# Performance work log

Measured on AMD Instinct MI355X. Metric: run time of the kernel, lower is better.

## Reference

```python
import jax, jax.numpy as jnp
import numpy as np

DIM = 1024
NUM_HEADS = 16


def setup_inputs() -> dict:
    key = jax.random.key(0)
    ks = jax.random.split(key, 8)
    B, N, C = 2, 2048, DIM
    x = jax.random.normal(ks[0], (B, N, C), dtype=jnp.float32)
    attn_mask = jnp.zeros((B, 1, N, N), dtype=jnp.float32)
    # learned parameters
    w_qkv = jax.random.normal(ks[1], (3 * C, C), dtype=jnp.float32) * (C ** -0.5)
    q_bias = jnp.zeros((C,), dtype=jnp.float32)
    k_bias = jnp.zeros((C,), dtype=jnp.float32)
    v_bias = jnp.zeros((C,), dtype=jnp.float32)
    w_proj = jax.random.normal(ks[2], (C, C), dtype=jnp.float32) * (C ** -0.5)
    b_proj = jnp.zeros((C,), dtype=jnp.float32)
    return {
        "x": x, "attn_mask": attn_mask,
        "w_qkv": w_qkv, "q_bias": q_bias, "k_bias": k_bias, "v_bias": v_bias,
        "w_proj": w_proj, "b_proj": b_proj,
        "num_heads": NUM_HEADS,
    }


def reference(x, attn_mask, w_qkv, q_bias, k_bias, v_bias, w_proj, b_proj, num_heads):
    B, N, C = x.shape
    H = num_heads
    hd = C // H
    scale = hd ** -0.5
    alpha = 32.0
    # fused qkv projection with concatenated biases
    qkv_bias = jnp.concatenate([q_bias, k_bias, v_bias])
    qkv = x @ w_qkv.T + qkv_bias                       # [B, N, 3C]
    qkv = qkv.reshape(B, N, 3, H, hd).transpose(2, 0, 3, 1, 4)  # [3, B, H, N, hd]
    q, k, v = qkv[0], qkv[1], qkv[2]
    # stabilization trick: scale q down by alpha, compute scores, re-scale after max-subtraction
    q = q * (scale / alpha)
    attn = jnp.einsum('bhld,bhmd->bhlm', q, k)         # [B, H, N, N]
    attn = (attn - jnp.max(attn, axis=-1, keepdims=True)) * alpha
    attn = attn + attn_mask                            # additive mask, broadcast over heads
    attn = jax.nn.softmax(attn, axis=-1)
    out = jnp.einsum('bhlm,bhmd->blhd', attn, v).reshape(B, N, C)
    out = out @ w_proj.T + b_proj
    return out
```

## Files before the change

### kernel.cpp

```cpp
#include <hip/hip_runtime.h>

typedef unsigned short u16;
typedef __bf16   bf16x8 __attribute__((ext_vector_type(8)));
typedef float    f32x4  __attribute__((ext_vector_type(4)));
typedef float    f32x16 __attribute__((ext_vector_type(16)));
typedef unsigned u32x4v __attribute__((ext_vector_type(4)));
typedef u16      u16x8  __attribute__((ext_vector_type(8)));

#define DEV __device__ __forceinline__

DEV u16 tobf(float f) {
  return __builtin_bit_cast(unsigned short, (__bf16)f);
}

DEV unsigned pack2(float a, float b) {
  return (unsigned)tobf(a) | ((unsigned)tobf(b) << 16);
}

DEV f32x4 fzero() { f32x4 z; z[0]=0.f; z[1]=0.f; z[2]=0.f; z[3]=0.f; return z; }

DEV void async_cp16(void* lds, const void* g) {
  __builtin_amdgcn_global_load_lds(
      (const __attribute__((address_space(1))) void*)g,
      (__attribute__((address_space(3))) void*)lds, 16, 0, 0);
}

DEV void cvt8(const float* __restrict__ in, u16* __restrict__ out, int i) {
  const float4* in4 = (const float4*)in;
  float4 a = in4[2*i], b = in4[2*i+1];
  u16x8 r;
  r[0]=tobf(a.x); r[1]=tobf(a.y); r[2]=tobf(a.z); r[3]=tobf(a.w);
  r[4]=tobf(b.x); r[5]=tobf(b.y); r[6]=tobf(b.z); r[7]=tobf(b.w);
  *(u16x8*)(out + 8*(size_t)i) = r;
}

__global__ void k_zero_flag(unsigned* f) {
  if (threadIdx.x == 0 && blockIdx.x == 0) *f = 0u;
}

__global__ __launch_bounds__(256)
void k_pre(const float* __restrict__ x, const float* __restrict__ wqkv,
           const float* __restrict__ wproj,
           u16* __restrict__ xb, u16* __restrict__ wqkvb, u16* __restrict__ wprojb,
           const u32x4v* __restrict__ mask, unsigned* __restrict__ flag)
{
  const int tid = blockIdx.x * blockDim.x + threadIdx.x;
  const int stride = gridDim.x * blockDim.x;
  for (int i = tid; i < 524288; i += stride) cvt8(x, xb, i);
  for (int i = tid; i < 393216; i += stride) cvt8(wqkv, wqkvb, i);
  for (int i = tid; i < 131072; i += stride) cvt8(wproj, wprojb, i);
  unsigned o = 0;
  for (int i = tid; i < 2097152; i += stride) {
    u32x4v v = mask[i];
    o |= v[0] | v[1] | v[2] | v[3];
  }
  if (o & 0x7fffffffu) atomicOr(flag, 1u);
}

template<int EPI>
__global__ __launch_bounds__(256)
void k_gemm_nt(const u16* __restrict__ A, const u16* __restrict__ B,
               int N, int K, int nbn,
               const float* __restrict__ bq, const float* __restrict__ bk,
               const float* __restrict__ bv,
               u16* __restrict__ qo, u16* __restrict__ ko, u16* __restrict__ vto,
               float* __restrict__ fo, const float* __restrict__ bp)
{
  __shared__ u16 sA[2][4096];
  __shared__ u16 sB[2][4096];

  const int tid  = threadIdx.x;
  const int lane = tid & 63;
  const int wave = tid >> 6;
  const int lr = lane & 15, lg = lane >> 4;
  const int wr = wave >> 1, wc = wave & 1;

  const int per = gridDim.x >> 3;
  const int bid = blockIdx.x;
  const int swz = (bid & 7) * per + (bid >> 3);
  const int bm0 = (swz / nbn) << 7;
  const int bn0 = (swz - (swz / nbn) * nbn) << 7;

  const size_t Kb = (size_t)K * 2;

  auto stage = [&](int buf, int kt) {
#pragma unroll
    for (int j = 0; j < 2; ++j) {
      int off = (tid + j * 256) << 4;
      int row = off >> 6;
      int ch  = (off & 63) >> 4;
      int gch = ch ^ (row & 3);
      async_cp16((char*)&sA[buf][0] + off,
                 (const char*)A + (size_t)(bm0 + row) * Kb + (size_t)kt * 64 + gch * 16);
      async_cp16((char*)&sB[buf][0] + off,
                 (const char*)B + (size_t)(bn0 + row) * Kb + (size_t)kt * 64 + gch * 16);
    }
  };

  f32x4 acc[4][4];
#pragma unroll
  for (int i = 0; i < 4; ++i)
#pragma unroll
    for (int j = 0; j < 4; ++j) acc[i][j] = fzero();

  const int nk = K >> 5;
  stage(0, 0);
  __syncthreads();

  for (int kt = 0; kt < nk; ++kt) {
    const int cur = kt & 1;
    if (kt + 1 < nk) stage(cur ^ 1, kt + 1);

    bf16x8 af[4], bfr[4];
#pragma unroll
    for (int mi = 0; mi < 4; ++mi) {
      int row = (wr << 6) + (mi << 4) + lr;
      int addr = (row << 6) + ((lg ^ (row & 3)) << 4);
      af[mi] = *(const bf16x8*)((const char*)&sA[cur][0] + addr);
    }
#pragma unroll
    for (int ni = 0; ni < 4; ++ni) {
      int row = (wc << 6) + (ni << 4) + lr;
      int addr = (row << 6) + ((lg ^ (row & 3)) << 4);
      bfr[ni] = *(const bf16x8*)((const char*)&sB[cur][0] + addr);
    }
#pragma unroll
    for (int mi = 0; mi < 4; ++mi)
#pragma unroll
      for (int ni = 0; ni < 4; ++ni)
        acc[mi][ni] = __builtin_amdgcn_mfma_f32_16x16x32_bf16(af[mi], bfr[ni], acc[mi][ni], 0, 0, 0);

    __syncthreads();
  }

#pragma unroll
  for (int mi = 0; mi < 4; ++mi) {
#pragma unroll
    for (int ni = 0; ni < 4; ++ni) {
      int col = bn0 + (wc << 6) + (ni << 4) + lr;
      if (EPI == 0) {
        int s = col >> 10, hd = col & 1023;
        int h = hd >> 6, d = hd & 63;
        float bias = (s == 0 ? bq[hd] : (s == 1 ? bk[hd] : bv[hd]));
#pragma unroll
        for (int r = 0; r < 4; ++r) {
          int m = bm0 + (wr << 6) + (mi << 4) + (lg << 2) + r;
          int b = m >> 11, n = m & 2047;
          float v = acc[mi][ni][r] + bias;
          if (s == 0) v *= 0.125f;
          u16 val = tobf(v);
          size_t bh = (size_t)(b * 16 + h);
          if (s == 0)      qo[(bh * 2048 + n) * 64 + d] = val;
          else if (s == 1) ko[(bh * 2048 + n) * 64 + d] = val;
          else             vto[(bh * 64 + d) * 2048 + n] = val;
        }
      } else {
        float bias = bp[col];
#pragma unroll
        for (int r = 0; r < 4; ++r) {
          int m = bm0 + (wr << 6) + (mi << 4) + (lg << 2) + r;
          fo[(size_t)m * N + col] = acc[mi][ni][r] + bias;
        }
      }
    }
  }
}

__global__ __launch_bounds__(256)
void k_attn(const u16* __restrict__ qb, const u16* __restrict__ kb,
            const u16* __restrict__ vtb, u16* __restrict__ ao,
            const float* __restrict__ mask, const unsigned* __restrict__ flag)
{
  constexpr int N = 2048;
  __shared__ u16 sK[2][4096];
  __shared__ u16 sV[2][4096];

  const int tid  = threadIdx.x;
  const int lane = tid & 63;
  const int wave = tid >> 6;
  const int l31  = lane & 31;
  const int hi   = lane >> 5;

  const int bid  = blockIdx.x;
  const int xcd  = bid & 7, slot = bid >> 3;
  const int bh   = xcd + 8 * (slot >> 4);
  const int qt   = slot & 15;
  const int b    = bh >> 4, h = bh & 15;

  const u16* Kbh = kb  + (size_t)bh * N * 64;
  const u16* Vbh = vtb + (size_t)bh * 64 * N;
  const int q_lo = qt * 128 + wave * 32;
  const int qg   = q_lo + l31;

  bf16x8 qf[4];
  {
    const u16* qrow = qb + ((size_t)bh * N + qg) * 64;
#pragma unroll
    for (int ks = 0; ks < 4; ++ks)
      qf[ks] = *(const bf16x8*)(qrow + ks * 16 + hi * 8);
  }

  const unsigned use_mask = *flag;
  const float* maskb = mask + (size_t)b * N * N;

  float m_run = -INFINITY, lsum = 0.f;
  f32x16 o0, o1;
#pragma unroll
  for (int r = 0; r < 16; ++r) { o0[r] = 0.f; o1[r] = 0.f; }

  auto stage = [&](int buf, int kt) {
#pragma unroll
    for (int j = 0; j < 2; ++j) {
      int off = (tid + j * 256) << 4;
      int row = off >> 7;
      int ch  = (off & 127) >> 4;
      int gch = ch ^ (row & 7);
      async_cp16((char*)&sK[buf][0] + off,
                 (const char*)Kbh + (size_t)(kt * 64 + row) * 128 + gch * 16);
      async_cp16((char*)&sV[buf][0] + off,
                 (const char*)Vbh + (size_t)row * (N * 2) + (size_t)kt * 128 + gch * 16);
    }
  };

  stage(0, 0);
  __syncthreads();

  const float L2E = 1.44269504088896340736f;

  for (int kt = 0; kt < N / 64; ++kt) {
    const int cur = kt & 1;
    if (kt + 1 < N / 64) stage(cur ^ 1, kt + 1);

    f32x16 sc0, sc1;
#pragma unroll
    for (int r = 0; r < 16; ++r) { sc0[r] = 0.f; sc1[r] = 0.f; }

    __builtin_amdgcn_s_setprio(1);
#pragma unroll
    for (int ks = 0; ks < 4; ++ks) {
      int row0 = l31;
      int a0 = (row0 << 7) + ((((ks << 1) + hi) ^ (row0 & 7)) << 4);
      bf16x8 kf0 = *(const bf16x8*)((const char*)&sK[cur][0] + a0);
      sc0 = __builtin_amdgcn_mfma_f32_32x32x16_bf16(kf0, qf[ks], sc0, 0, 0, 0);
      int row1 = 32 + l31;
      int a1 = (row1 << 7) + ((((ks << 1) + hi) ^ (row1 & 7)) << 4);
      bf16x8 kf1 = *(const bf16x8*)((const char*)&sK[cur][0] + a1);
      sc1 = __builtin_amdgcn_mfma_f32_32x32x16_bf16(kf1, qf[ks], sc1, 0, 0, 0);
    }
    __builtin_amdgcn_s_setprio(0);

    if (use_mask) {
#pragma unroll
      for (int r = 0; r < 16; ++r) {
        int krow = (r & 3) + 8 * (r >> 2) + 4 * hi;
        sc0[r] += maskb[(size_t)qg * N + kt * 64 + krow];
        sc1[r] += maskb[(size_t)qg * N + kt * 64 + 32 + krow];
      }
    }

    float t[8];
#pragma unroll
    for (int r = 0; r < 8; ++r)
      t[r] = fmaxf(fmaxf(sc0[r], sc0[r + 8]), fmaxf(sc1[r], sc1[r + 8]));
#pragma unroll
    for (int r = 0; r < 4; ++r) t[r] = fmaxf(t[r], t[r + 4]);
    float pm = fmaxf(fmaxf(t[0], t[1]), fmaxf(t[2], t[3]));
    pm = fmaxf(pm, __shfl_xor(pm, 32, 64));

    if (__any(pm > m_run + 8.f)) {
      const float m_new = fmaxf(m_run, pm);
      const float f = __builtin_amdgcn_exp2f((m_run - m_new) * L2E);
      m_run = m_new;
      float fr[16];
#pragma unroll
      for (int r = 0; r < 16; ++r)
        fr[r] = __shfl(f, (r & 3) + 8 * (r >> 2) + 4 * hi, 64);
#pragma unroll
      for (int r = 0; r < 16; ++r) { o0[r] *= fr[r]; o1[r] *= fr[r]; }
      lsum *= f;
    }

    const float mL2 = m_run * L2E;
    float rs0 = 0.f, rs1 = 0.f, rs2 = 0.f, rs3 = 0.f;
#pragma unroll
    for (int r = 0; r < 16; r += 4) {
      sc0[r]   = __builtin_amdgcn_exp2f(__builtin_fmaf(sc0[r],   L2E, -mL2));
      sc0[r+1] = __builtin_amdgcn_exp2f(__builtin_fmaf(sc0[r+1], L2E, -mL2));
      sc0[r+2] = __builtin_amdgcn_exp2f(__builtin_fmaf(sc0[r+2], L2E, -mL2));
      sc0[r+3] = __builtin_amdgcn_exp2f(__builtin_fmaf(sc0[r+3], L2E, -mL2));
      sc1[r]   = __builtin_amdgcn_exp2f(__builtin_fmaf(sc1[r],   L2E, -mL2));
      sc1[r+1] = __builtin_amdgcn_exp2f(__builtin_fmaf(sc1[r+1], L2E, -mL2));
      sc1[r+2] = __builtin_amdgcn_exp2f(__builtin_fmaf(sc1[r+2], L2E, -mL2));
      sc1[r+3] = __builtin_amdgcn_exp2f(__builtin_fmaf(sc1[r+3], L2E, -mL2));
      rs0 += sc0[r]   + sc1[r];
      rs1 += sc0[r+1] + sc1[r+1];
      rs2 += sc0[r+2] + sc1[r+2];
      rs3 += sc0[r+3] + sc1[r+3];
    }
    float rs = (rs0 + rs1) + (rs2 + rs3);
    rs += __shfl_xor(rs, 32, 64);
    lsum += rs;

    unsigned P32_0[8], P32_1[8];
#pragma unroll
    for (int tt = 0; tt < 8; ++tt) {
      P32_0[tt] = pack2(sc0[2 * tt], sc0[2 * tt + 1]);
      P32_1[tt] = pack2(sc1[2 * tt], sc1[2 * tt + 1]);
    }

    bf16x8 pa[4];
#pragma unroll
    for (int ks16 = 0; ks16 < 4; ++ks16) {
      const int b4 = (ks16 & 1) << 2;
      unsigned c0, c1, c2, c3;
      if (ks16 < 2) { c0 = P32_0[b4]; c2 = P32_0[b4+2]; c1 = P32_0[b4+1]; c3 = P32_0[b4+3]; }
      else          { c0 = P32_1[b4]; c2 = P32_1[b4+2]; c1 = P32_1[b4+1]; c3 = P32_1[b4+3]; }
      asm volatile("v_permlane32_swap_b32 %0, %1" : "+v"(c0), "+v"(c2));
      asm volatile("v_permlane32_swap_b32 %0, %1" : "+v"(c1), "+v"(c3));
      u32x4v w; w[0] = c0; w[1] = c1; w[2] = c2; w[3] = c3;
      pa[ks16] = __builtin_bit_cast(bf16x8, w);
    }

    __builtin_amdgcn_s_setprio(1);
#pragma unroll
    for (int ks16 = 0; ks16 < 4; ++ks16) {
      int row0 = l31;
      int a0 = (row0 << 7) + ((((ks16 << 1) + hi) ^ (row0 & 7)) << 4);
      bf16x8 vf0 = *(const bf16x8*)((const char*)&sV[cur][0] + a0);
      o0 = __builtin_amdgcn_mfma_f32_32x32x16_bf16(pa[ks16], vf0, o0, 0, 0, 0);
      int row1 = 32 + l31;
      int a1 = (row1 << 7) + ((((ks16 << 1) + hi) ^ (row1 & 7)) << 4);
      bf16x8 vf1 = *(const bf16x8*)((const char*)&sV[cur][0] + a1);
      o1 = __builtin_amdgcn_mfma_f32_32x32x16_bf16(pa[ks16], vf1, o1, 0, 0, 0);
    }
    __builtin_amdgcn_s_setprio(0);

    __syncthreads();
  }

  const float inv = 1.0f / lsum;
  float ivr[16];
#pragma unroll
  for (int r = 0; r < 16; ++r)
    ivr[r] = __shfl(inv, (r & 3) + 8 * (r >> 2) + 4 * hi, 64);

#pragma unroll
  for (int r = 0; r < 16; ++r) {
    int qrow = q_lo + (r & 3) + 8 * (r >> 2) + 4 * hi;
    size_t base = ((size_t)(b * N + qrow)) * 1024 + h * 64;
    ao[base + l31]      = tobf(o0[r] * ivr[r]);
    ao[base + 32 + l31] = tobf(o1[r] * ivr[r]);
  }
}

extern "C" void kernel_launch(void* const* d_in, const int* in_sizes, int n_in,
                              void* d_out, int out_size, void* d_ws, size_t ws_size,
                              hipStream_t stream) {
  const float* x      = (const float*)d_in[0];
  const float* mask   = (const float*)d_in[1];
  const float* w_qkv  = (const float*)d_in[2];
  const float* q_bias = (const float*)d_in[3];
  const float* k_bias = (const float*)d_in[4];
  const float* v_bias = (const float*)d_in[5];
  const float* w_proj = (const float*)d_in[6];
  const float* b_proj = (const float*)d_in[7];
  float* out = (float*)d_out;

  const int B = 2, N = 2048, C = 1024;
  const int M = B * N;

  u16* ws     = (u16*)d_ws;
  u16* xb     = ws;
  u16* wqkvb  = ws + 4194304;
  u16* wprojb = ws + 7340032;
  u16* qbuf   = ws + 8388608;
  u16* kbuf   = ws + 12582912;
  u16* vtbuf  = ws + 16777216;
  unsigned* flag = (unsigned*)(ws + 20971520);
  u16* aob    = xb;

  k_zero_flag<<<1, 64, 0, stream>>>(flag);
  k_pre<<<2048, 256, 0, stream>>>(x, w_qkv, w_proj, xb, wqkvb, wprojb,
                                  (const u32x4v*)mask, flag);

  k_gemm_nt<0><<<(M / 128) * (3 * C / 128), 256, 0, stream>>>(
      xb, wqkvb, 3 * C, C, 3 * C / 128,
      q_bias, k_bias, v_bias, qbuf, kbuf, vtbuf, nullptr, nullptr);

  k_attn<<<B * 16 * (N / 128), 256, 0, stream>>>(qbuf, kbuf, vtbuf, aob, mask, flag);

  k_gemm_nt<1><<<(M / 128) * (C / 128), 256, 0, stream>>>(
      aob, wprojb, C, C, C / 128,
      nullptr, nullptr, nullptr, nullptr, nullptr, nullptr, out, b_proj);
}
```

Before: 143.1 us.

## Split KV loop across two wave groups per block and merge softmax partials

Attention blocks now use 512 threads as two groups of four waves, each processing alternating 64-key tiles with their own double-buffered K/V shared memory. At the end, group 1 writes its running max, sum and output accumulators to shared memory and group 0 merges them with rescaling before writing bf16 output. This aims to raise waves per CU and halve the sequential key loop length per wave, at the cost of doubled LDS usage and an extra merge step.

```diff
diff --git a/kernel.cpp b/kernel.cpp
--- a/kernel.cpp
+++ b/kernel.cpp
@@ -166,18 +166,22 @@
   }
 }
 
-__global__ __launch_bounds__(256)
+__global__ __launch_bounds__(512, 4)
 void k_attn(const u16* __restrict__ qb, const u16* __restrict__ kb,
             const u16* __restrict__ vtb, u16* __restrict__ ao,
             const float* __restrict__ mask, const unsigned* __restrict__ flag)
 {
   constexpr int N = 2048;
-  __shared__ u16 sK[2][4096];
-  __shared__ u16 sV[2][4096];
+  __shared__ u16 sK[2][2][4096];
+  __shared__ u16 sV[2][2][4096];
+  __shared__ float2 sStats[256];
 
   const int tid  = threadIdx.x;
   const int lane = tid & 63;
   const int wave = tid >> 6;
+  const int g    = wave >> 2;
+  const int wq   = wave & 3;
+  const int ltid = tid & 255;
   const int l31  = lane & 31;
   const int hi   = lane >> 5;
 
@@ -189,7 +193,7 @@
 
   const u16* Kbh = kb  + (size_t)bh * N * 64;
   const u16* Vbh = vtb + (size_t)bh * 64 * N;
-  const int q_lo = qt * 128 + wave * 32;
+  const int q_lo = qt * 128 + wq * 32;
   const int qg   = q_lo + l31;
 
   bf16x8 qf[4];
@@ -211,25 +215,29 @@
   auto stage = [&](int buf, int kt) {
 #pragma unroll
     for (int j = 0; j < 2; ++j) {
-      int off = (tid + j * 256) << 4;
+      int off = (ltid + j * 256) << 4;
       int row = off >> 7;
       int ch  = (off & 127) >> 4;
       int gch = ch ^ (row & 7);
-      async_cp16((char*)&sK[buf][0] + off,
+      async_cp16((char*)&sK[g][buf][0] + off,
                  (const char*)Kbh + (size_t)(kt * 64 + row) * 128 + gch * 16);
-      async_cp16((char*)&sV[buf][0] + off,
+      async_cp16((char*)&sV[g][buf][0] + off,
                  (const char*)Vbh + (size_t)row * (N * 2) + (size_t)kt * 128 + gch * 16);
     }
   };
 
-  stage(0, 0);
+  stage(0, g);
   __syncthreads();
 
   const float L2E = 1.44269504088896340736f;
 
-  for (int kt = 0; kt < N / 64; ++kt) {
-    const int cur = kt & 1;
-    if (kt + 1 < N / 64) stage(cur ^ 1, kt + 1);
+  for (int t = 0; t < 16; ++t) {
+    const int kt  = 2 * t + g;
+    const int cur = t & 1;
+    if (t + 1 < 16) stage(cur ^ 1, kt + 2);
+
+    const char* kbase = (const char*)&sK[g][cur][0];
+    const char* vbase = (const char*)&sV[g][cur][0];
 
     f32x16 sc0, sc1;
 #pragma unroll
@@ -240,11 +248,11 @@
     for (int ks = 0; ks < 4; ++ks) {
       int row0 = l31;
       int a0 = (row0 << 7) + ((((ks << 1) + hi) ^ (row0 & 7)) << 4);
-      bf16x8 kf0 = *(const bf16x8*)((const char*)&sK[cur][0] + a0);
+      bf16x8 kf0 = *(const bf16x8*)(kbase + a0);
       sc0 = __builtin_amdgcn_mfma_f32_32x32x16_bf16(kf0, qf[ks], sc0, 0, 0, 0);
       int row1 = 32 + l31;
       int a1 = (row1 << 7) + ((((ks << 1) + hi) ^ (row1 & 7)) << 4);
-      bf16x8 kf1 = *(const bf16x8*)((const char*)&sK[cur][0] + a1);
+      bf16x8 kf1 = *(const bf16x8*)(kbase + a1);
       sc1 = __builtin_amdgcn_mfma_f32_32x32x16_bf16(kf1, qf[ks], sc1, 0, 0, 0);
     }
     __builtin_amdgcn_s_setprio(0);
@@ -258,13 +266,13 @@
       }
     }
 
-    float t[8];
+    float tmx[8];
 #pragma unroll
     for (int r = 0; r < 8; ++r)
-      t[r] = fmaxf(fmaxf(sc0[r], sc0[r + 8]), fmaxf(sc1[r], sc1[r + 8]));
-#pragma unroll
-    for (int r = 0; r < 4; ++r) t[r] = fmaxf(t[r], t[r + 4]);
-    float pm = fmaxf(fmaxf(t[0], t[1]), fmaxf(t[2], t[3]));
+      tmx[r] = fmaxf(fmaxf(sc0[r], sc0[r + 8]), fmaxf(sc1[r], sc1[r + 8]));
+#pragma unroll
+    for (int r = 0; r < 4; ++r) tmx[r] = fmaxf(tmx[r], tmx[r + 4]);
+    float pm = fmaxf(fmaxf(tmx[0], tmx[1]), fmaxf(tmx[2], tmx[3]));
     pm = fmaxf(pm, __shfl_xor(pm, 32, 64));
 
     if (__any(pm > m_run + 8.f)) {
@@ -326,11 +334,11 @@
     for (int ks16 = 0; ks16 < 4; ++ks16) {
       int row0 = l31;
       int a0 = (row0 << 7) + ((((ks16 << 1) + hi) ^ (row0 & 7)) << 4);
-      bf16x8 vf0 = *(const bf16x8*)((const char*)&sV[cur][0] + a0);
+      bf16x8 vf0 = *(const bf16x8*)(vbase + a0);
       o0 = __builtin_amdgcn_mfma_f32_32x32x16_bf16(pa[ks16], vf0, o0, 0, 0, 0);
       int row1 = 32 + l31;
       int a1 = (row1 << 7) + ((((ks16 << 1) + hi) ^ (row1 & 7)) << 4);
-      bf16x8 vf1 = *(const bf16x8*)((const char*)&sV[cur][0] + a1);
+      bf16x8 vf1 = *(const bf16x8*)(vbase + a1);
       o1 = __builtin_amdgcn_mfma_f32_32x32x16_bf16(pa[ks16], vf1, o1, 0, 0, 0);
     }
     __builtin_amdgcn_s_setprio(0);
@@ -338,18 +346,47 @@
     __syncthreads();
   }
 
-  const float inv = 1.0f / lsum;
-  float ivr[16];
-#pragma unroll
-  for (int r = 0; r < 16; ++r)
-    ivr[r] = __shfl(inv, (r & 3) + 8 * (r >> 2) + 4 * hi, 64);
-
-#pragma unroll
-  for (int r = 0; r < 16; ++r) {
-    int qrow = q_lo + (r & 3) + 8 * (r >> 2) + 4 * hi;
-    size_t base = ((size_t)(b * N + qrow)) * 1024 + h * 64;
-    ao[base + l31]      = tobf(o0[r] * ivr[r]);
-    ao[base + 32 + l31] = tobf(o1[r] * ivr[r]);
+  const int sw = lane & 7;
+  {
+    float* R = (wq < 2) ? ((float*)&sK[1][0][0] + ((wq & 1) * 64 + lane) * 32)
+                        : ((float*)&sV[1][0][0] + ((wq & 1) * 64 + lane) * 32);
+    if (g == 1) {
+      sStats[wq * 64 + lane] = make_float2(m_run, lsum);
+#pragma unroll
+      for (int i = 0; i < 4; ++i) {
+        f32x4 tv; tv[0]=o0[4*i]; tv[1]=o0[4*i+1]; tv[2]=o0[4*i+2]; tv[3]=o0[4*i+3];
+        *(f32x4*)(R + 4 * (i ^ sw)) = tv;
+      }
+#pragma unroll
+      for (int i = 0; i < 4; ++i) {
+        f32x4 tv; tv[0]=o1[4*i]; tv[1]=o1[4*i+1]; tv[2]=o1[4*i+2]; tv[3]=o1[4*i+3];
+        *(f32x4*)(R + 4 * ((i + 4) ^ sw)) = tv;
+      }
+    }
+    __syncthreads();
+    if (g == 0) {
+      float2 s1 = sStats[wq * 64 + lane];
+      float mf = fmaxf(m_run, s1.x);
+      float ea = __builtin_amdgcn_exp2f((m_run - mf) * L2E);
+      float eb = __builtin_amdgcn_exp2f((s1.x  - mf) * L2E);
+      float lf = __builtin_fmaf(lsum, ea, s1.y * eb);
+      float ai = ea / lf, bi = eb / lf;
+      f32x4 c[8];
+#pragma unroll
+      for (int i = 0; i < 8; ++i) c[i] = *(const f32x4*)(R + 4 * (i ^ sw));
+#pragma unroll
+      for (int r = 0; r < 16; ++r) {
+        int idx = (r & 3) + 8 * (r >> 2) + 4 * hi;
+        float Ar = __shfl(ai, idx, 64);
+        float Br = __shfl(bi, idx, 64);
+        float v0 = __builtin_fmaf(o0[r], Ar, c[r >> 2][r & 3] * Br);
+        float v1 = __builtin_fmaf(o1[r], Ar, c[4 + (r >> 2)][r & 3] * Br);
+        int qrow = q_lo + idx;
+        size_t base = ((size_t)(b * N + qrow)) * 1024 + h * 64;
+        ao[base + l31]      = tobf(v0);
+        ao[base + 32 + l31] = tobf(v1);
+      }
+    }
   }
 }
 
@@ -387,7 +424,7 @@
       xb, wqkvb, 3 * C, C, 3 * C / 128,
       q_bias, k_bias, v_bias, qbuf, kbuf, vtbuf, nullptr, nullptr);
 
-  k_attn<<<B * 16 * (N / 128), 256, 0, stream>>>(qbuf, kbuf, vtbuf, aob, mask, flag);
+  k_attn<<<B * 16 * (N / 128), 512, 0, stream>>>(qbuf, kbuf, vtbuf, aob, mask, flag);
 
   k_gemm_nt<1><<<(M / 128) * (C / 128), 256, 0, stream>>>(
       aob, wprojb, C, C, C / 128,
```

After: 144.7 us. Within noise of the previous version (+1.1%).

## Restructure attention into single-wave blocks with 32-key tiles and no barriers

Applied to the files above, without the earlier changes.

The attention kernel now uses one 64-thread wave per block, each owning 32 query rows. It streams 32-key tiles through double-buffered LDS with a new swizzle for the half-width V tile, and syncs with explicit vmcnt waits instead of __syncthreads. The aim is to remove block-level barrier stalls and raise the number of independent waves. In exchange, K/V reuse across query tiles within a block is lost, global and L2 traffic rises, and each tile issues fewer MFMAs between synchronisation points. The flag-zeroing kernel is also replaced by hipMemsetAsync.

```diff
diff --git a/kernel.cpp b/kernel.cpp
--- a/kernel.cpp
+++ b/kernel.cpp
@@ -32,10 +32,6 @@
   r[0]=tobf(a.x); r[1]=tobf(a.y); r[2]=tobf(a.z); r[3]=tobf(a.w);
   r[4]=tobf(b.x); r[5]=tobf(b.y); r[6]=tobf(b.z); r[7]=tobf(b.w);
   *(u16x8*)(out + 8*(size_t)i) = r;
-}
-
-__global__ void k_zero_flag(unsigned* f) {
-  if (threadIdx.x == 0 && blockIdx.x == 0) *f = 0u;
 }
 
 __global__ __launch_bounds__(256)
@@ -166,30 +162,29 @@
   }
 }
 
-__global__ __launch_bounds__(256)
+__global__ __launch_bounds__(64)
 void k_attn(const u16* __restrict__ qb, const u16* __restrict__ kb,
             const u16* __restrict__ vtb, u16* __restrict__ ao,
             const float* __restrict__ mask, const unsigned* __restrict__ flag)
 {
   constexpr int N = 2048;
-  __shared__ u16 sK[2][4096];
-  __shared__ u16 sV[2][4096];
-
-  const int tid  = threadIdx.x;
-  const int lane = tid & 63;
-  const int wave = tid >> 6;
+  constexpr int NT = N / 32;
+  __shared__ u16 sK[2][2048];
+  __shared__ u16 sV[2][2048];
+
+  const int lane = threadIdx.x & 63;
   const int l31  = lane & 31;
   const int hi   = lane >> 5;
 
   const int bid  = blockIdx.x;
   const int xcd  = bid & 7, slot = bid >> 3;
-  const int bh   = xcd + 8 * (slot >> 4);
-  const int qt   = slot & 15;
+  const int qt   = slot >> 2;
+  const int bh   = xcd + 8 * (slot & 3);
   const int b    = bh >> 4, h = bh & 15;
 
-  const u16* Kbh = kb  + (size_t)bh * N * 64;
-  const u16* Vbh = vtb + (size_t)bh * 64 * N;
-  const int q_lo = qt * 128 + wave * 32;
+  const char* Kb8 = (const char*)(kb  + (size_t)bh * N * 64);
+  const char* Vb8 = (const char*)(vtb + (size_t)bh * 64 * N);
+  const int q_lo = qt * 32;
   const int qg   = q_lo + l31;
 
   bf16x8 qf[4];
@@ -210,42 +205,51 @@
 
   auto stage = [&](int buf, int kt) {
 #pragma unroll
-    for (int j = 0; j < 2; ++j) {
-      int off = (tid + j * 256) << 4;
+    for (int j = 0; j < 4; ++j) {
+      int off = (lane + j * 64) << 4;
       int row = off >> 7;
       int ch  = (off & 127) >> 4;
       int gch = ch ^ (row & 7);
       async_cp16((char*)&sK[buf][0] + off,
-                 (const char*)Kbh + (size_t)(kt * 64 + row) * 128 + gch * 16);
+                 Kb8 + (size_t)(kt * 32 + row) * 128 + gch * 16);
+    }
+#pragma unroll
+    for (int j = 0; j < 4; ++j) {
+      int off = (lane + j * 64) << 4;
+      int row = off >> 6;
+      int ch  = (off & 63) >> 4;
+      int gch = ch ^ ((row >> 1) & 3);
       async_cp16((char*)&sV[buf][0] + off,
-                 (const char*)Vbh + (size_t)row * (N * 2) + (size_t)kt * 128 + gch * 16);
+                 Vb8 + (size_t)row * (N * 2) + kt * 64 + gch * 16);
     }
   };
 
   stage(0, 0);
-  __syncthreads();
 
   const float L2E = 1.44269504088896340736f;
 
-  for (int kt = 0; kt < N / 64; ++kt) {
-    const int cur = kt & 1;
-    if (kt + 1 < N / 64) stage(cur ^ 1, kt + 1);
-
-    f32x16 sc0, sc1;
-#pragma unroll
-    for (int r = 0; r < 16; ++r) { sc0[r] = 0.f; sc1[r] = 0.f; }
-
+  for (int t = 0; t < NT; ++t) {
+    const int cur = t & 1;
+    if (t + 1 < NT) {
+      stage(cur ^ 1, t + 1);
+      asm volatile("s_waitcnt vmcnt(8)" ::: "memory");
+    } else {
+      asm volatile("s_waitcnt vmcnt(0)" ::: "memory");
+    }
+    __builtin_amdgcn_sched_barrier(0);
+
+    const char* kbase = (const char*)&sK[cur][0];
+    const char* vbase = (const char*)&sV[cur][0];
+
+    f32x16 sc;
+#pragma unroll
+    for (int r = 0; r < 16; ++r) sc[r] = 0.f;
     __builtin_amdgcn_s_setprio(1);
 #pragma unroll
     for (int ks = 0; ks < 4; ++ks) {
-      int row0 = l31;
-      int a0 = (row0 << 7) + ((((ks << 1) + hi) ^ (row0 & 7)) << 4);
-      bf16x8 kf0 = *(const bf16x8*)((const char*)&sK[cur][0] + a0);
-      sc0 = __builtin_amdgcn_mfma_f32_32x32x16_bf16(kf0, qf[ks], sc0, 0, 0, 0);
-      int row1 = 32 + l31;
-      int a1 = (row1 << 7) + ((((ks << 1) + hi) ^ (row1 & 7)) << 4);
-      bf16x8 kf1 = *(const bf16x8*)((const char*)&sK[cur][0] + a1);
-      sc1 = __builtin_amdgcn_mfma_f32_32x32x16_bf16(kf1, qf[ks], sc1, 0, 0, 0);
+      int a0 = (l31 << 7) + ((((ks << 1) + hi) ^ (l31 & 7)) << 4);
+      bf16x8 kf = *(const bf16x8*)(kbase + a0);
+      sc = __builtin_amdgcn_mfma_f32_32x32x16_bf16(kf, qf[ks], sc, 0, 0, 0);
     }
     __builtin_amdgcn_s_setprio(0);
 
@@ -253,30 +257,27 @@
 #pragma unroll
       for (int r = 0; r < 16; ++r) {
         int krow = (r & 3) + 8 * (r >> 2) + 4 * hi;
-        sc0[r] += maskb[(size_t)qg * N + kt * 64 + krow];
-        sc1[r] += maskb[(size_t)qg * N + kt * 64 + 32 + krow];
+        sc[r] += maskb[(size_t)qg * N + t * 32 + krow];
       }
     }
 
-    float t[8];
-#pragma unroll
-    for (int r = 0; r < 8; ++r)
-      t[r] = fmaxf(fmaxf(sc0[r], sc0[r + 8]), fmaxf(sc1[r], sc1[r + 8]));
-#pragma unroll
-    for (int r = 0; r < 4; ++r) t[r] = fmaxf(t[r], t[r + 4]);
-    float pm = fmaxf(fmaxf(t[0], t[1]), fmaxf(t[2], t[3]));
+    float tm[8];
+#pragma unroll
+    for (int r = 0; r < 8; ++r) tm[r] = fmaxf(sc[r], sc[r + 8]);
+#pragma unroll
+    for (int r = 0; r < 4; ++r) tm[r] = fmaxf(tm[r], tm[r + 4]);
+    float pm = fmaxf(fmaxf(tm[0], tm[1]), fmaxf(tm[2], tm[3]));
     pm = fmaxf(pm, __shfl_xor(pm, 32, 64));
 
     if (__any(pm > m_run + 8.f)) {
       const float m_new = fmaxf(m_run, pm);
       const float f = __builtin_amdgcn_exp2f((m_run - m_new) * L2E);
       m_run = m_new;
-      float fr[16];
-#pragma unroll
-      for (int r = 0; r < 16; ++r)
-        fr[r] = __shfl(f, (r & 3) + 8 * (r >> 2) + 4 * hi, 64);
-#pragma unroll
-      for (int r = 0; r < 16; ++r) { o0[r] *= fr[r]; o1[r] *= fr[r]; }
+#pragma unroll
+      for (int r = 0; r < 16; ++r) {
+        float fr = __shfl(f, (r & 3) + 8 * (r >> 2) + 4 * hi, 64);
+        o0[r] *= fr; o1[r] *= fr;
+      }
       lsum *= f;
     }
 
@@ -284,37 +285,26 @@
     float rs0 = 0.f, rs1 = 0.f, rs2 = 0.f, rs3 = 0.f;
 #pragma unroll
     for (int r = 0; r < 16; r += 4) {
-      sc0[r]   = __builtin_amdgcn_exp2f(__builtin_fmaf(sc0[r],   L2E, -mL2));
-      sc0[r+1] = __builtin_amdgcn_exp2f(__builtin_fmaf(sc0[r+1], L2E, -mL2));
-      sc0[r+2] = __builtin_amdgcn_exp2f(__builtin_fmaf(sc0[r+2], L2E, -mL2));
-      sc0[r+3] = __builtin_amdgcn_exp2f(__builtin_fmaf(sc0[r+3], L2E, -mL2));
-      sc1[r]   = __builtin_amdgcn_exp2f(__builtin_fmaf(sc1[r],   L2E, -mL2));
-      sc1[r+1] = __builtin_amdgcn_exp2f(__builtin_fmaf(sc1[r+1], L2E, -mL2));
-      sc1[r+2] = __builtin_amdgcn_exp2f(__builtin_fmaf(sc1[r+2], L2E, -mL2));
-      sc1[r+3] = __builtin_amdgcn_exp2f(__builtin_fmaf(sc1[r+3], L2E, -mL2));
-      rs0 += sc0[r]   + sc1[r];
-      rs1 += sc0[r+1] + sc1[r+1];
-      rs2 += sc0[r+2] + sc1[r+2];
-      rs3 += sc0[r+3] + sc1[r+3];
+      sc[r]   = __builtin_amdgcn_exp2f(__builtin_fmaf(sc[r],   L2E, -mL2));
+      sc[r+1] = __builtin_amdgcn_exp2f(__builtin_fmaf(sc[r+1], L2E, -mL2));
+      sc[r+2] = __builtin_amdgcn_exp2f(__builtin_fmaf(sc[r+2], L2E, -mL2));
+      sc[r+3] = __builtin_amdgcn_exp2f(__builtin_fmaf(sc[r+3], L2E, -mL2));
+      rs0 += sc[r]; rs1 += sc[r+1]; rs2 += sc[r+2]; rs3 += sc[r+3];
     }
     float rs = (rs0 + rs1) + (rs2 + rs3);
     rs += __shfl_xor(rs, 32, 64);
     lsum += rs;
 
-    unsigned P32_0[8], P32_1[8];
-#pragma unroll
-    for (int tt = 0; tt < 8; ++tt) {
-      P32_0[tt] = pack2(sc0[2 * tt], sc0[2 * tt + 1]);
-      P32_1[tt] = pack2(sc1[2 * tt], sc1[2 * tt + 1]);
-    }
-
-    bf16x8 pa[4];
-#pragma unroll
-    for (int ks16 = 0; ks16 < 4; ++ks16) {
-      const int b4 = (ks16 & 1) << 2;
-      unsigned c0, c1, c2, c3;
-      if (ks16 < 2) { c0 = P32_0[b4]; c2 = P32_0[b4+2]; c1 = P32_0[b4+1]; c3 = P32_0[b4+3]; }
-      else          { c0 = P32_1[b4]; c2 = P32_1[b4+2]; c1 = P32_1[b4+1]; c3 = P32_1[b4+3]; }
+    unsigned P32[8];
+#pragma unroll
+    for (int tt = 0; tt < 8; ++tt)
+      P32[tt] = pack2(sc[2 * tt], sc[2 * tt + 1]);
+
+    bf16x8 pa[2];
+#pragma unroll
+    for (int ks16 = 0; ks16 < 2; ++ks16) {
+      const int b4 = ks16 << 2;
+      unsigned c0 = P32[b4], c2 = P32[b4 + 2], c1 = P32[b4 + 1], c3 = P32[b4 + 3];
       asm volatile("v_permlane32_swap_b32 %0, %1" : "+v"(c0), "+v"(c2));
       asm volatile("v_permlane32_swap_b32 %0, %1" : "+v"(c1), "+v"(c3));
       u32x4v w; w[0] = c0; w[1] = c1; w[2] = c2; w[3] = c3;
@@ -323,33 +313,27 @@
 
     __builtin_amdgcn_s_setprio(1);
 #pragma unroll
-    for (int ks16 = 0; ks16 < 4; ++ks16) {
-      int row0 = l31;
-      int a0 = (row0 << 7) + ((((ks16 << 1) + hi) ^ (row0 & 7)) << 4);
-      bf16x8 vf0 = *(const bf16x8*)((const char*)&sV[cur][0] + a0);
+    for (int ks16 = 0; ks16 < 2; ++ks16) {
+      int a0 = (l31 << 6) + ((((ks16 << 1) + hi) ^ ((l31 >> 1) & 3)) << 4);
+      bf16x8 vf0 = *(const bf16x8*)(vbase + a0);
       o0 = __builtin_amdgcn_mfma_f32_32x32x16_bf16(pa[ks16], vf0, o0, 0, 0, 0);
       int row1 = 32 + l31;
-      int a1 = (row1 << 7) + ((((ks16 << 1) + hi) ^ (row1 & 7)) << 4);
-      bf16x8 vf1 = *(const bf16x8*)((const char*)&sV[cur][0] + a1);
+      int a1 = (row1 << 6) + ((((ks16 << 1) + hi) ^ ((row1 >> 1) & 3)) << 4);
+      bf16x8 vf1 = *(const bf16x8*)(vbase + a1);
       o1 = __builtin_amdgcn_mfma_f32_32x32x16_bf16(pa[ks16], vf1, o1, 0, 0, 0);
     }
     __builtin_amdgcn_s_setprio(0);
-
-    __syncthreads();
   }
 
   const float inv = 1.0f / lsum;
-  float ivr[16];
-#pragma unroll
-  for (int r = 0; r < 16; ++r)
-    ivr[r] = __shfl(inv, (r & 3) + 8 * (r >> 2) + 4 * hi, 64);
-
 #pragma unroll
   for (int r = 0; r < 16; ++r) {
-    int qrow = q_lo + (r & 3) + 8 * (r >> 2) + 4 * hi;
+    int idx = (r & 3) + 8 * (r >> 2) + 4 * hi;
+    float ivr = __shfl(inv, idx, 64);
+    int qrow = q_lo + idx;
     size_t base = ((size_t)(b * N + qrow)) * 1024 + h * 64;
-    ao[base + l31]      = tobf(o0[r] * ivr[r]);
-    ao[base + 32 + l31] = tobf(o1[r] * ivr[r]);
+    ao[base + l31]      = tobf(o0[r] * ivr);
+    ao[base + 32 + l31] = tobf(o1[r] * ivr);
   }
 }
 
@@ -379,7 +363,7 @@
   unsigned* flag = (unsigned*)(ws + 20971520);
   u16* aob    = xb;
 
-  k_zero_flag<<<1, 64, 0, stream>>>(flag);
+  hipMemsetAsync(flag, 0, 4, stream);
   k_pre<<<2048, 256, 0, stream>>>(x, w_qkv, w_proj, xb, wqkvb, wprojb,
                                   (const u32x4v*)mask, flag);
 
@@ -387,7 +371,7 @@
       xb, wqkvb, 3 * C, C, 3 * C / 128,
       q_bias, k_bias, v_bias, qbuf, kbuf, vtbuf, nullptr, nullptr);
 
-  k_attn<<<B * 16 * (N / 128), 256, 0, stream>>>(qbuf, kbuf, vtbuf, aob, mask, flag);
+  k_attn<<<B * 16 * (N / 32), 64, 0, stream>>>(qbuf, kbuf, vtbuf, aob, mask, flag);
 
   k_gemm_nt<1><<<(M / 128) * (C / 128), 256, 0, stream>>>(
       aob, wprojb, C, C, C / 128,
```

Result: slower. 163.7 us (+14.4%).

## Deepen attention K/V pipeline to four buffers with explicit vmcnt waits

Applied to the files above, without the earlier changes.

The attention kernel moves from double to quad-buffered K/V tiles in LDS, prefetching two tiles ahead and replacing the per-iteration __syncthreads with explicit vmcnt waits and a single barrier. The GEMM kernel likewise uses manual vmcnt waits and raw barriers, and raises wave priority around its MFMA block. The flag-zeroing kernel is replaced by hipMemsetAsync. The aim is to hide global-to-LDS latency and cut barrier overhead, at the cost of doubled LDS use in attention, which may reduce occupancy, and fragile hand-counted wait values.

```diff
diff --git a/kernel.cpp b/kernel.cpp
--- a/kernel.cpp
+++ b/kernel.cpp
@@ -32,10 +32,6 @@
   r[0]=tobf(a.x); r[1]=tobf(a.y); r[2]=tobf(a.z); r[3]=tobf(a.w);
   r[4]=tobf(b.x); r[5]=tobf(b.y); r[6]=tobf(b.z); r[7]=tobf(b.w);
   *(u16x8*)(out + 8*(size_t)i) = r;
-}
-
-__global__ void k_zero_flag(unsigned* f) {
-  if (threadIdx.x == 0 && blockIdx.x == 0) *f = 0u;
 }
 
 __global__ __launch_bounds__(256)
@@ -105,11 +101,17 @@
 
   const int nk = K >> 5;
   stage(0, 0);
-  __syncthreads();
 
   for (int kt = 0; kt < nk; ++kt) {
     const int cur = kt & 1;
-    if (kt + 1 < nk) stage(cur ^ 1, kt + 1);
+    if (kt + 1 < nk) {
+      stage(cur ^ 1, kt + 1);
+      asm volatile("s_waitcnt vmcnt(4)" ::: "memory");
+    } else {
+      asm volatile("s_waitcnt vmcnt(0)" ::: "memory");
+    }
+    __builtin_amdgcn_s_barrier();
+    __builtin_amdgcn_sched_barrier(0);
 
     bf16x8 af[4], bfr[4];
 #pragma unroll
@@ -124,13 +126,15 @@
       int addr = (row << 6) + ((lg ^ (row & 3)) << 4);
       bfr[ni] = *(const bf16x8*)((const char*)&sB[cur][0] + addr);
     }
+    __builtin_amdgcn_s_setprio(1);
 #pragma unroll
     for (int mi = 0; mi < 4; ++mi)
 #pragma unroll
       for (int ni = 0; ni < 4; ++ni)
         acc[mi][ni] = __builtin_amdgcn_mfma_f32_16x16x32_bf16(af[mi], bfr[ni], acc[mi][ni], 0, 0, 0);
-
-    __syncthreads();
+    __builtin_amdgcn_s_setprio(0);
+
+    __builtin_amdgcn_s_barrier();
   }
 
 #pragma unroll
@@ -172,8 +176,9 @@
             const float* __restrict__ mask, const unsigned* __restrict__ flag)
 {
   constexpr int N = 2048;
-  __shared__ u16 sK[2][4096];
-  __shared__ u16 sV[2][4096];
+  constexpr int NTT = N / 64;
+  __shared__ u16 sK[4][4096];
+  __shared__ u16 sV[4][4096];
 
   const int tid  = threadIdx.x;
   const int lane = tid & 63;
@@ -223,13 +228,21 @@
   };
 
   stage(0, 0);
-  __syncthreads();
+  stage(1, 1);
 
   const float L2E = 1.44269504088896340736f;
 
-  for (int kt = 0; kt < N / 64; ++kt) {
-    const int cur = kt & 1;
-    if (kt + 1 < N / 64) stage(cur ^ 1, kt + 1);
+  for (int kt = 0; kt < NTT; ++kt) {
+    const int cur = kt & 3;
+    if (kt + 2 < NTT) stage((kt + 2) & 3, kt + 2);
+    if (kt + 2 < NTT)      asm volatile("s_waitcnt vmcnt(8)" ::: "memory");
+    else if (kt + 1 < NTT) asm volatile("s_waitcnt vmcnt(4)" ::: "memory");
+    else                   asm volatile("s_waitcnt vmcnt(0)" ::: "memory");
+    __builtin_amdgcn_s_barrier();
+    __builtin_amdgcn_sched_barrier(0);
+
+    const char* kbase = (const char*)&sK[cur][0];
+    const char* vbase = (const char*)&sV[cur][0];
 
     f32x16 sc0, sc1;
 #pragma unroll
@@ -240,11 +253,11 @@
     for (int ks = 0; ks < 4; ++ks) {
       int row0 = l31;
       int a0 = (row0 << 7) + ((((ks << 1) + hi) ^ (row0 & 7)) << 4);
-      bf16x8 kf0 = *(const bf16x8*)((const char*)&sK[cur][0] + a0);
+      bf16x8 kf0 = *(const bf16x8*)(kbase + a0);
       sc0 = __builtin_amdgcn_mfma_f32_32x32x16_bf16(kf0, qf[ks], sc0, 0, 0, 0);
       int row1 = 32 + l31;
       int a1 = (row1 << 7) + ((((ks << 1) + hi) ^ (row1 & 7)) << 4);
-      bf16x8 kf1 = *(const bf16x8*)((const char*)&sK[cur][0] + a1);
+      bf16x8 kf1 = *(const bf16x8*)(kbase + a1);
       sc1 = __builtin_amdgcn_mfma_f32_32x32x16_bf16(kf1, qf[ks], sc1, 0, 0, 0);
     }
     __builtin_amdgcn_s_setprio(0);
@@ -258,25 +271,24 @@
       }
     }
 
-    float t[8];
+    float tmx[8];
 #pragma unroll
     for (int r = 0; r < 8; ++r)
-      t[r] = fmaxf(fmaxf(sc0[r], sc0[r + 8]), fmaxf(sc1[r], sc1[r + 8]));
-#pragma unroll
-    for (int r = 0; r < 4; ++r) t[r] = fmaxf(t[r], t[r + 4]);
-    float pm = fmaxf(fmaxf(t[0], t[1]), fmaxf(t[2], t[3]));
+      tmx[r] = fmaxf(fmaxf(sc0[r], sc0[r + 8]), fmaxf(sc1[r], sc1[r + 8]));
+#pragma unroll
+    for (int r = 0; r < 4; ++r) tmx[r] = fmaxf(tmx[r], tmx[r + 4]);
+    float pm = fmaxf(fmaxf(tmx[0], tmx[1]), fmaxf(tmx[2], tmx[3]));
     pm = fmaxf(pm, __shfl_xor(pm, 32, 64));
 
     if (__any(pm > m_run + 8.f)) {
       const float m_new = fmaxf(m_run, pm);
       const float f = __builtin_amdgcn_exp2f((m_run - m_new) * L2E);
       m_run = m_new;
-      float fr[16];
-#pragma unroll
-      for (int r = 0; r < 16; ++r)
-        fr[r] = __shfl(f, (r & 3) + 8 * (r >> 2) + 4 * hi, 64);
-#pragma unroll
-      for (int r = 0; r < 16; ++r) { o0[r] *= fr[r]; o1[r] *= fr[r]; }
+#pragma unroll
+      for (int r = 0; r < 16; ++r) {
+        float fr = __shfl(f, (r & 3) + 8 * (r >> 2) + 4 * hi, 64);
+        o0[r] *= fr; o1[r] *= fr;
+      }
       lsum *= f;
     }
 
@@ -326,30 +338,25 @@
     for (int ks16 = 0; ks16 < 4; ++ks16) {
       int row0 = l31;
       int a0 = (row0 << 7) + ((((ks16 << 1) + hi) ^ (row0 & 7)) << 4);
-      bf16x8 vf0 = *(const bf16x8*)((const char*)&sV[cur][0] + a0);
+      bf16x8 vf0 = *(const bf16x8*)(vbase + a0);
       o0 = __builtin_amdgcn_mfma_f32_32x32x16_bf16(pa[ks16], vf0, o0, 0, 0, 0);
       int row1 = 32 + l31;
       int a1 = (row1 << 7) + ((((ks16 << 1) + hi) ^ (row1 & 7)) << 4);
-      bf16x8 vf1 = *(const bf16x8*)((const char*)&sV[cur][0] + a1);
+      bf16x8 vf1 = *(const bf16x8*)(vbase + a1);
       o1 = __builtin_amdgcn_mfma_f32_32x32x16_bf16(pa[ks16], vf1, o1, 0, 0, 0);
     }
     __builtin_amdgcn_s_setprio(0);
-
-    __syncthreads();
   }
 
   const float inv = 1.0f / lsum;
-  float ivr[16];
-#pragma unroll
-  for (int r = 0; r < 16; ++r)
-    ivr[r] = __shfl(inv, (r & 3) + 8 * (r >> 2) + 4 * hi, 64);
-
 #pragma unroll
   for (int r = 0; r < 16; ++r) {
-    int qrow = q_lo + (r & 3) + 8 * (r >> 2) + 4 * hi;
+    int idx = (r & 3) + 8 * (r >> 2) + 4 * hi;
+    float ivr = __shfl(inv, idx, 64);
+    int qrow = q_lo + idx;
     size_t base = ((size_t)(b * N + qrow)) * 1024 + h * 64;
-    ao[base + l31]      = tobf(o0[r] * ivr[r]);
-    ao[base + 32 + l31] = tobf(o1[r] * ivr[r]);
+    ao[base + l31]      = tobf(o0[r] * ivr);
+    ao[base + 32 + l31] = tobf(o1[r] * ivr);
   }
 }
 
@@ -379,7 +386,7 @@
   unsigned* flag = (unsigned*)(ws + 20971520);
   u16* aob    = xb;
 
-  k_zero_flag<<<1, 64, 0, stream>>>(flag);
+  hipMemsetAsync(flag, 0, 4, stream);
   k_pre<<<2048, 256, 0, stream>>>(x, w_qkv, w_proj, xb, wqkvb, wprojb,
                                   (const u32x4v*)mask, flag);
 
```

New measurement: 144.0 us. About the same (+0.6%).
